# Optimization experiments

Hardware: AMD Instinct MI355X
Metric: run time of the kernel (lower is better)

## Reference

```python
import jax, jax.numpy as jnp
import numpy as np

B, N, D = 16, 512, 512
H, DH = 8, 64
INNER = H * DH            # attention inner dim = 512
FF = 4 * D                # feedforward hidden = 2048
CI = 2 * D                # conv expansion inner = 1024
K = 31                    # depthwise kernel
MAXPOS = 512
EPS = 1e-5                # LayerNorm / BatchNorm eps (torch defaults)
PAD = (K // 2, K // 2 - (K + 1) % 2)  # calc_same_padding(31) -> (15, 15)


def _ln(x, g, b):
    m = x.mean(-1, keepdims=True)
    v = ((x - m) ** 2).mean(-1, keepdims=True)
    return (x - m) / jnp.sqrt(v + EPS) * g + b


def _swish(x):
    return x * jax.nn.sigmoid(x)


def setup_inputs() -> dict:
    key = jax.random.key(0)
    ks = jax.random.split(key, 16)
    s = 0.02
    inp = {
        'x': jax.random.normal(ks[0], (B, N, D), jnp.float32),
        # FF1
        'ff1_ln_g': jnp.ones((D,), jnp.float32), 'ff1_ln_b': jnp.zeros((D,), jnp.float32),
        'ff1_w1': jax.random.normal(ks[1], (D, FF), jnp.float32) * s,
        'ff1_b1': jnp.zeros((FF,), jnp.float32),
        'ff1_w2': jax.random.normal(ks[2], (FF, D), jnp.float32) * s,
        'ff1_b2': jnp.zeros((D,), jnp.float32),
        # Attention
        'attn_ln_g': jnp.ones((D,), jnp.float32), 'attn_ln_b': jnp.zeros((D,), jnp.float32),
        'qkv_w': jax.random.normal(ks[3], (D, 3 * INNER), jnp.float32) * s,
        'out_w': jax.random.normal(ks[4], (INNER, D), jnp.float32) * s,
        'rel_emb': jax.random.normal(ks[5], (2 * MAXPOS + 1, DH), jnp.float32) * s,
        # Conv module
        'conv_ln_g': jnp.ones((D,), jnp.float32), 'conv_ln_b': jnp.zeros((D,), jnp.float32),
        'pw1_w': jax.random.normal(ks[6], (2 * CI, D), jnp.float32) * s,
        'pw1_b': jnp.zeros((2 * CI,), jnp.float32),
        'dw_w': jax.random.normal(ks[7], (CI, 1, K), jnp.float32) * s,
        'dw_b': jnp.zeros((CI,), jnp.float32),
        'bn_g': jnp.ones((CI,), jnp.float32), 'bn_b': jnp.zeros((CI,), jnp.float32),
        'bn_mean': jnp.zeros((CI,), jnp.float32), 'bn_var': jnp.ones((CI,), jnp.float32),
        'pw2_w': jax.random.normal(ks[8], (D, CI), jnp.float32) * s,
        'pw2_b': jnp.zeros((D,), jnp.float32),
        # FF2
        'ff2_ln_g': jnp.ones((D,), jnp.float32), 'ff2_ln_b': jnp.zeros((D,), jnp.float32),
        'ff2_w1': jax.random.normal(ks[9], (D, FF), jnp.float32) * s,
        'ff2_b1': jnp.zeros((FF,), jnp.float32),
        'ff2_w2': jax.random.normal(ks[10], (FF, D), jnp.float32) * s,
        'ff2_b2': jnp.zeros((D,), jnp.float32),
        # post norm
        'post_ln_g': jnp.ones((D,), jnp.float32), 'post_ln_b': jnp.zeros((D,), jnp.float32),
    }
    return inp


def _ff(x, g, b, w1, b1, w2, b2):
    h = _ln(x, g, b)
    h = _swish(h @ w1 + b1)
    return h @ w2 + b2


def _attention(x, g, b, qkv_w, out_w, rel_emb):
    n = x.shape[1]
    scale = DH ** (-0.5)
    h = _ln(x, g, b)
    qkv = h @ qkv_w                                    # [b,n,3*inner]
    q, k, v = jnp.split(qkv, 3, axis=-1)
    q = q.reshape(B, n, H, DH).transpose(0, 2, 1, 3)   # [b,h,n,d]
    k = k.reshape(B, n, H, DH).transpose(0, 2, 1, 3)
    v = v.reshape(B, n, H, DH).transpose(0, 2, 1, 3)
    dots = jnp.einsum('bhnd,bhmd->bhnm', q, k) * scale
    seq = jnp.arange(n)
    dist = jnp.clip(seq[:, None] - seq[None, :], -MAXPOS, MAXPOS) + MAXPOS  # [n,n]
    rpe = rel_emb[dist]                                # [n,r,d]
    pos = jnp.einsum('bhnd,nrd->bhnr', q, rpe) * scale
    sim = dots + pos
    attn = jax.nn.softmax(sim.astype(jnp.float32), axis=-1).astype(q.dtype)
    out = jnp.einsum('bhnm,bhmd->bhnd', attn, v)
    out = out.transpose(0, 2, 1, 3).reshape(B, n, INNER)
    return out @ out_w


def _conv_module(x, ln_g, ln_b, pw1_w, pw1_b, dw_w, dw_b, bn_g, bn_b, bn_mean, bn_var, pw2_w, pw2_b):
    h = _ln(x, ln_g, ln_b)                             # [b,n,c]
    h = h.transpose(0, 2, 1)                           # [b,c,n]
    h = jnp.einsum('oc,bcn->bon', pw1_w, h) + pw1_b[:, None]  # pointwise conv1 -> [b,2ci,n]
    out, gate = jnp.split(h, 2, axis=1)
    h = out * jax.nn.sigmoid(gate)                     # GLU -> [b,ci,n]
    h = jnp.pad(h, ((0, 0), (0, 0), PAD))
    h = jax.lax.conv_general_dilated(
        h, dw_w, window_strides=(1,), padding='VALID',
        feature_group_count=CI, dimension_numbers=('NCH', 'OIH', 'NCH'))
    h = h + dw_b[:, None]
    # BatchNorm1d eval-mode with running stats
    h = (h - bn_mean[:, None]) / jnp.sqrt(bn_var[:, None] + EPS) * bn_g[:, None] + bn_b[:, None]
    h = _swish(h)
    h = jnp.einsum('oc,bcn->bon', pw2_w, h) + pw2_b[:, None]  # pointwise conv2 -> [b,d,n]
    return h.transpose(0, 2, 1)


def reference(x, ff1_ln_g, ff1_ln_b, ff1_w1, ff1_b1, ff1_w2, ff1_b2,
              attn_ln_g, attn_ln_b, qkv_w, out_w, rel_emb,
              conv_ln_g, conv_ln_b, pw1_w, pw1_b, dw_w, dw_b,
              bn_g, bn_b, bn_mean, bn_var, pw2_w, pw2_b,
              ff2_ln_g, ff2_ln_b, ff2_w1, ff2_b1, ff2_w2, ff2_b2,
              post_ln_g, post_ln_b):
    x = 0.5 * _ff(x, ff1_ln_g, ff1_ln_b, ff1_w1, ff1_b1, ff1_w2, ff1_b2) + x
    x = _attention(x, attn_ln_g, attn_ln_b, qkv_w, out_w, rel_emb) + x
    x = _conv_module(x, conv_ln_g, conv_ln_b, pw1_w, pw1_b, dw_w, dw_b,
                     bn_g, bn_b, bn_mean, bn_var, pw2_w, pw2_b) + x
    x = 0.5 * _ff(x, ff2_ln_g, ff2_ln_b, ff2_w1, ff2_b1, ff2_w2, ff2_b2) + x
    return _ln(x, post_ln_g, post_ln_b)
```

## Files before the change

kernel.cpp:

```cpp
#include <hip/hip_runtime.h>
#include <stdint.h>

#define ROWS 8192
#define N_ 512

typedef __attribute__((ext_vector_type(4))) float f32x4;
typedef __attribute__((ext_vector_type(8))) short s16x8;
typedef __attribute__((ext_vector_type(4))) short s16x4;
typedef __attribute__((ext_vector_type(8))) unsigned short u16x8;

__device__ __forceinline__ float bf2f(unsigned short h){
  union { unsigned int u; float f; } v; v.u = ((unsigned int)h) << 16; return v.f;
}
__device__ __forceinline__ unsigned short f2bf(float f){
  union { float f; unsigned int u; } v; v.f = f;
  unsigned int r = v.u + 0x7FFFu + ((v.u >> 16) & 1u);
  return (unsigned short)(r >> 16);
}
__device__ __forceinline__ float sigm(float x){ return 1.f / (1.f + __expf(-x)); }
__device__ __forceinline__ unsigned cvtpk(float lo, float hi){
  unsigned r;
  asm("v_cvt_pk_bf16_f32 %0, %1, %2" : "=v"(r) : "v"(lo), "v"(hi));
  return r;
}

__global__ void k_transpose_cvt(const float* __restrict__ in, unsigned short* __restrict__ out,
                                int R, int C){
  __shared__ float t[32][33];
  int c0 = blockIdx.x*32, r0 = blockIdx.y*32;
  int tx = threadIdx.x & 31, ty = threadIdx.x >> 5;
  #pragma unroll
  for(int i=0;i<32;i+=8) t[ty+i][tx] = in[(size_t)(r0+ty+i)*C + c0+tx];
  __syncthreads();
  #pragma unroll
  for(int i=0;i<32;i+=8) out[(size_t)(c0+ty+i)*R + r0+tx] = f2bf(t[tx][ty+i]);
}

__global__ void k_cvt(const float* __restrict__ in, unsigned short* __restrict__ out, int n){
  int i = blockIdx.x*256 + threadIdx.x;
  if(i < n) out[i] = f2bf(in[i]);
}

__global__ void k_vtrans(const unsigned short* __restrict__ qkv, unsigned short* __restrict__ vt){
  __shared__ unsigned short t[64][72];
  const int tid = threadIdx.x;
  const int n0 = blockIdx.x * 64;
  const int bh = blockIdx.y;
  const int b = bh >> 3, h = bh & 7;
  #pragma unroll
  for(int i=0;i<2;i++){
    int flat = i*256 + tid;
    int tok = flat >> 3, c = flat & 7;
    u16x8 v = *(const u16x8*)(qkv + (size_t)(b*N_ + n0 + tok)*1536 + 1024 + h*64 + c*8);
    *(u16x8*)(&t[tok][c*8]) = v;
  }
  __syncthreads();
  #pragma unroll
  for(int i=0;i<2;i++){
    int flat = i*256 + tid;
    int d = flat >> 3, tc = flat & 7;
    u16x8 o;
    #pragma unroll
    for(int e=0;e<8;e++) o[e] = t[tc*8+e][d];
    *(u16x8*)(vt + (((size_t)bh*64 + d) << 9) + n0 + tc*8) = o;
  }
}

template<int OUTF32>
__global__ void k_ln(const float* __restrict__ x, const float* __restrict__ gw,
                     const float* __restrict__ bw, void* __restrict__ outp){
  const int row = blockIdx.x*4 + (threadIdx.x >> 6);
  const int lane = threadIdx.x & 63;
  const f32x4* xr = (const f32x4*)(x + (size_t)row*512);
  f32x4 v0 = xr[lane], v1 = xr[lane + 64];
  float s  = v0[0]+v0[1]+v0[2]+v0[3] + v1[0]+v1[1]+v1[2]+v1[3];
  float s2 = v0[0]*v0[0]+v0[1]*v0[1]+v0[2]*v0[2]+v0[3]*v0[3]
           + v1[0]*v1[0]+v1[1]*v1[1]+v1[2]*v1[2]+v1[3]*v1[3];
  #pragma unroll
  for(int off=1; off<64; off<<=1){ s += __shfl_xor(s, off); s2 += __shfl_xor(s2, off); }
  float mean = s * (1.f/512.f);
  float inv = rsqrtf(s2*(1.f/512.f) - mean*mean + 1e-5f);
  const f32x4* gv = (const f32x4*)gw; const f32x4* bv = (const f32x4*)bw;
  f32x4 g0 = gv[lane], g1 = gv[lane+64], b0 = bv[lane], b1 = bv[lane+64];
  f32x4 o0, o1;
  #pragma unroll
  for(int e=0;e<4;e++){ o0[e] = (v0[e]-mean)*inv*g0[e] + b0[e];
                        o1[e] = (v1[e]-mean)*inv*g1[e] + b1[e]; }
  if(OUTF32){
    f32x4* op = (f32x4*)((float*)outp + (size_t)row*512);
    op[lane] = o0; op[lane+64] = o1;
  } else {
    unsigned short* ob = (unsigned short*)outp + (size_t)row*512;
    s16x4 h0, h1;
    #pragma unroll
    for(int e=0;e<4;e++){ h0[e] = (short)f2bf(o0[e]); h1[e] = (short)f2bf(o1[e]); }
    *(s16x4*)(ob + lane*4) = h0;
    *(s16x4*)(ob + 256 + lane*4) = h1;
  }
}

template<int EPI>
__global__ __launch_bounds__(256, 2)
void k_gemm(const unsigned short* __restrict__ A, const unsigned short* __restrict__ Bt,
            const float* __restrict__ bias, const float* __restrict__ res,
            void* __restrict__ outp, int M, int N, int K){
  __shared__ unsigned short As[128*64];
  __shared__ unsigned short Bs[128*64];
  const int tid = threadIdx.x, lane = tid & 63, wave = tid >> 6;
  const int nwg = gridDim.x * gridDim.y;
  int orig = blockIdx.x + gridDim.x * blockIdx.y;
  int q8 = nwg >> 3, r8 = nwg & 7, xcd = orig & 7, idx = orig >> 3;
  int wg = (xcd < r8 ? xcd * (q8 + 1) : r8 * (q8 + 1) + (xcd - r8) * q8) + idx;
  const int m0 = (wg / gridDim.x) * 128, n0 = (wg % gridDim.x) * 128;
  const int wm = (wave >> 1) * 64, wn = (wave & 1) * 64;
  f32x4 acc[4][4];
  #pragma unroll
  for(int a=0;a<4;a++)
    #pragma unroll
    for(int b=0;b<4;b++) acc[a][b] = (f32x4){0.f,0.f,0.f,0.f};

  for(int kt = 0; kt < K; kt += 64){
    #pragma unroll
    for(int i=0;i<4;i++){
      int flat = i*256 + tid;
      int r = flat >> 3, c = flat & 7;
      int dst = r*64 + ((c ^ (r & 7)) << 3);
      *(u16x8*)(&As[dst]) = *(const u16x8*)(A + (size_t)(m0 + r)*K + kt + c*8);
      *(u16x8*)(&Bs[dst]) = *(const u16x8*)(Bt + (size_t)(n0 + r)*K + kt + c*8);
    }
    __syncthreads();
    #pragma unroll
    for(int ks=0; ks<2; ks++){
      s16x8 af[4], bfr[4];
      #pragma unroll
      for(int mi=0;mi<4;mi++){
        int row = wm + mi*16 + (lane & 15);
        int ch = (ks*4 + (lane >> 4)) ^ (row & 7);
        af[mi] = *(const s16x8*)(&As[row*64 + ch*8]);
      }
      #pragma unroll
      for(int ni=0;ni<4;ni++){
        int row = wn + ni*16 + (lane & 15);
        int ch = (ks*4 + (lane >> 4)) ^ (row & 7);
        bfr[ni] = *(const s16x8*)(&Bs[row*64 + ch*8]);
      }
      #pragma unroll
      for(int mi=0;mi<4;mi++)
        #pragma unroll
        for(int ni=0;ni<4;ni++)
          acc[mi][ni] = __builtin_amdgcn_mfma_f32_16x16x32_bf16(af[mi], bfr[ni], acc[mi][ni], 0, 0, 0);
    }
    __syncthreads();
  }
  const int rb = (lane >> 4) * 4, cb = lane & 15;
  #pragma unroll
  for(int mi=0;mi<4;mi++){
    #pragma unroll
    for(int ni=0;ni<4;ni++){
      int col = n0 + wn + ni*16 + cb;
      #pragma unroll
      for(int r=0;r<4;r++){
        int row = m0 + wm + mi*16 + rb + r;
        float v = acc[mi][ni][r];
        if(EPI==1||EPI==2||EPI==4||EPI==5) v += bias[col];
        if(EPI==2) v = 0.5f*v + res[(size_t)row*N + col];
        if(EPI==3||EPI==5) v += res[(size_t)row*N + col];
        if(EPI==1) v = v * sigm(v);
        if(EPI==0||EPI==1||EPI==4) ((unsigned short*)outp)[(size_t)row*N + col] = f2bf(v);
        else                        ((float*)outp)[(size_t)row*N + col] = v;
      }
    }
  }
}

__global__ __launch_bounds__(256, 2)
void k_attn(const unsigned short* __restrict__ qkv, const unsigned short* __restrict__ vt,
            const unsigned short* __restrict__ emb, unsigned short* __restrict__ outb){
  __shared__ unsigned short KV[512*64];
  const int tid = threadIdx.x, lane = tid & 63, w = tid >> 6;
  const int q0 = blockIdx.x * 64, h = blockIdx.y, b = blockIdx.z;
  const int j = lane & 15, g = lane >> 4;
  const int n0w = q0 + w*16;
  const size_t qkvbase = (size_t)b*N_*1536;

  #pragma unroll
  for(int i=0;i<16;i++){
    int flat = i*256 + tid;
    int r = flat >> 3, c = flat & 7;
    *(u16x8*)(&KV[r*64 + ((c ^ (r & 7)) << 3)]) =
      *(const u16x8*)(qkv + qkvbase + (size_t)r*1536 + 512 + h*64 + c*8);
  }
  s16x8 qf[2];
  #pragma unroll
  for(int ks=0;ks<2;ks++)
    qf[ks] = *(const s16x8*)(qkv + qkvbase + (size_t)(n0w + j)*1536 + h*64 + ks*32 + g*8);
  f32x4 pa1 = {0.f,0.f,0.f,0.f};
  #pragma unroll
  for(int ks=0;ks<2;ks++){
    s16x8 e1 = *(const s16x8*)(emb + (size_t)(n0w + 513 + j)*64 + ks*32 + g*8);
    pa1 = __builtin_amdgcn_mfma_f32_16x16x32_bf16(e1, qf[ks], pa1, 0,0,0);
  }
  __syncthreads();

  f32x4 sc[32];
  #pragma unroll
  for(int rt=0;rt<32;rt++){
    const int cb = n0w - rt*16 + 512;
    f32x4 s   = {0.f,0.f,0.f,0.f};
    f32x4 pa0 = {0.f,0.f,0.f,0.f};
    #pragma unroll
    for(int ks=0;ks<2;ks++){
      int row = rt*16 + j;
      int ch = (ks*4 + g) ^ (row & 7);
      s16x8 kf = *(const s16x8*)(&KV[row*64 + (ch<<3)]);
      s = __builtin_amdgcn_mfma_f32_16x16x32_bf16(kf, qf[ks], s, 0,0,0);
      s16x8 e0 = *(const s16x8*)(emb + (size_t)(cb - 15 + j)*64 + ks*32 + g*8);
      pa0 = __builtin_amdgcn_mfma_f32_16x16x32_bf16(e0, qf[ks], pa0, 0,0,0);
    }
    #pragma unroll
    for(int reg=0;reg<4;reg++){
      int elem = (j + 3 - reg) & 3;
      float s0 = (elem & 2) ? ((elem & 1) ? pa0[3] : pa0[2]) : ((elem & 1) ? pa0[1] : pa0[0]);
      float s1 = (elem & 2) ? ((elem & 1) ? pa1[3] : pa1[2]) : ((elem & 1) ? pa1[1] : pa1[0]);
      int m = j + 15 - g*4 - reg;
      int src = j + (((m & 15) >> 2) << 4);
      float v0 = __shfl(s0, src);
      float v1 = __shfl(s1, src);
      sc[rt][reg] = s[reg] + (m < 16 ? v0 : v1);
    }
    pa1 = pa0;
  }
  __syncthreads();

  #pragma unroll
  for(int i=0;i<16;i++){
    int flat = i*256 + tid;
    int d = flat >> 6, rc = flat & 63;
    u16x8 v = *(const u16x8*)(vt + (((size_t)(b*8 + h)*64 + d) << 9) + rc*8);
    *(u16x8*)(&KV[d*512 + ((rc ^ (d & 7)) << 3)]) = v;
  }

  const float C2 = 0.125f * 1.4426950408889634f;
  float mx = -1e30f;
  #pragma unroll
  for(int rt=0;rt<32;rt++)
    mx = fmaxf(mx, fmaxf(fmaxf(sc[rt][0], sc[rt][1]), fmaxf(sc[rt][2], sc[rt][3])));
  mx = fmaxf(mx, __shfl_xor(mx, 16));
  mx = fmaxf(mx, __shfl_xor(mx, 32));
  const float mc = mx * C2;
  float sm = 0.f;
  unsigned w0[32], w1[32];
  #pragma unroll
  for(int rt=0;rt<32;rt++){
    float p0 = exp2f(fmaf(sc[rt][0], C2, -mc));
    float p1 = exp2f(fmaf(sc[rt][1], C2, -mc));
    float p2 = exp2f(fmaf(sc[rt][2], C2, -mc));
    float p3 = exp2f(fmaf(sc[rt][3], C2, -mc));
    sm += (p0 + p1) + (p2 + p3);
    w0[rt] = cvtpk(p0, p1);
    w1[rt] = cvtpk(p2, p3);
  }
  sm += __shfl_xor(sm, 16);
  sm += __shfl_xor(sm, 32);
  float inv = 1.f / sm;
  __syncthreads();

  f32x4 o[4];
  #pragma unroll
  for(int dt=0;dt<4;dt++) o[dt] = (f32x4){0.f,0.f,0.f,0.f};
  const int srcA = j + ((g & 1) << 5);
  const int srcB = srcA + 16;
  const bool hi = (g >= 2);
  #pragma unroll
  for(int rts=0; rts<16; rts++){
    unsigned a0 = __shfl(w0[2*rts],   srcA);
    unsigned a1 = __shfl(w1[2*rts],   srcA);
    unsigned a2 = __shfl(w0[2*rts],   srcB);
    unsigned a3 = __shfl(w1[2*rts],   srcB);
    unsigned b0 = __shfl(w0[2*rts+1], srcA);
    unsigned b1 = __shfl(w1[2*rts+1], srcA);
    unsigned b2 = __shfl(w0[2*rts+1], srcB);
    unsigned b3 = __shfl(w1[2*rts+1], srcB);
    union { unsigned u[4]; s16x8 v; } pu;
    pu.u[0] = hi ? b0 : a0;
    pu.u[1] = hi ? b1 : a1;
    pu.u[2] = hi ? b2 : a2;
    pu.u[3] = hi ? b3 : a3;
    #pragma unroll
    for(int dt=0;dt<4;dt++){
      int d = dt*16 + j;
      int ch = (rts*4 + g) ^ (d & 7);
      s16x8 vf = *(const s16x8*)(&KV[d*512 + (ch<<3)]);
      o[dt] = __builtin_amdgcn_mfma_f32_16x16x32_bf16(pu.v, vf, o[dt], 0,0,0);
    }
  }
  #pragma unroll
  for(int reg=0;reg<4;reg++){
    float invq = __shfl(inv, (g<<2) + reg);
    int tok = n0w + (g<<2) + reg;
    #pragma unroll
    for(int dt=0;dt<4;dt++)
      outb[(size_t)(b*N_ + tok)*512 + h*64 + dt*16 + j] = f2bf(o[dt][reg] * invq);
  }
}

__global__ void k_glu(const unsigned short* __restrict__ hid, unsigned short* __restrict__ outp){
  size_t i = (size_t)blockIdx.x*256 + threadIdx.x;
  int row = (int)(i >> 7), cc = (int)(i & 127);
  u16x8 a  = *(const u16x8*)(hid + (size_t)row*2048 + cc*8);
  u16x8 gt = *(const u16x8*)(hid + (size_t)row*2048 + 1024 + cc*8);
  u16x8 o;
  #pragma unroll
  for(int e=0;e<8;e++){
    float av = bf2f(a[e]), gv = bf2f(gt[e]);
    o[e] = f2bf(av * sigm(gv));
  }
  *(u16x8*)(outp + (size_t)row*1024 + cc*8) = o;
}

__global__ __launch_bounds__(256, 2)
void k_dwconv(const unsigned short* __restrict__ gin, const float* __restrict__ dww,
              const float* __restrict__ dwb, const float* __restrict__ bng,
              const float* __restrict__ bnb, const float* __restrict__ bnm,
              const float* __restrict__ bnv, unsigned short* __restrict__ outp){
  __shared__ unsigned short gl[94][136];
  __shared__ float wl[31][128];
  const int c0 = blockIdx.x*128, n0 = blockIdx.y*64, b = blockIdx.z;
  const int tid = threadIdx.x;
  for(int i=0;i<6;i++){
    int flat = i*256 + tid;
    if(flat < 94*16){
      int r = flat >> 4, c = flat & 15;
      int n = n0 - 15 + r;
      u16x8 v = {0,0,0,0,0,0,0,0};
      if(n >= 0 && n < 512) v = *(const u16x8*)(gin + (size_t)(b*512 + n)*1024 + c0 + c*8);
      *(u16x8*)(&gl[r][c*8]) = v;
    }
  }
  for(int i=0;i<16;i++){
    int flat = i*256 + tid;
    if(flat < 31*128){
      int t = flat >> 7, cc = flat & 127;
      wl[t][cc] = dww[(size_t)(c0 + cc)*31 + t];
    }
  }
  __syncthreads();
  const int tc = tid & 31, tn = tid >> 5;
  f32x4 acc[8];
  #pragma unroll
  for(int nn=0;nn<8;nn++) acc[nn] = (f32x4){0.f,0.f,0.f,0.f};
  for(int t=0;t<31;t++){
    f32x4 wv = *(const f32x4*)(&wl[t][tc*4]);
    #pragma unroll
    for(int nn=0;nn<8;nn++){
      s16x4 gv = *(const s16x4*)(&gl[tn*8 + nn + t][tc*4]);
      f32x4 g4 = { bf2f((unsigned short)gv[0]), bf2f((unsigned short)gv[1]),
                   bf2f((unsigned short)gv[2]), bf2f((unsigned short)gv[3]) };
      acc[nn] += g4 * wv;
    }
  }
  #pragma unroll
  for(int e=0;e<4;e++){
    int c = c0 + tc*4 + e;
    float s  = bng[c] * rsqrtf(bnv[c] + 1e-5f);
    float sh = bnb[c] - bnm[c]*s;
    float db = dwb[c];
    #pragma unroll
    for(int nn=0;nn<8;nn++){
      float v = (acc[nn][e] + db)*s + sh;
      v = v * sigm(v);
      outp[(size_t)(b*512 + n0 + tn*8 + nn)*1024 + c] = f2bf(v);
    }
  }
}

extern "C" void kernel_launch(void* const* d_in, const int* in_sizes, int n_in,
                              void* d_out, int out_size, void* d_ws, size_t ws_size,
                              hipStream_t stream){
  const float* x        = (const float*)d_in[0];
  const float* ff1_ln_g = (const float*)d_in[1];
  const float* ff1_ln_b = (const float*)d_in[2];
  const float* ff1_w1   = (const float*)d_in[3];
  const float* ff1_b1   = (const float*)d_in[4];
  const float* ff1_w2   = (const float*)d_in[5];
  const float* ff1_b2   = (const float*)d_in[6];
  const float* attn_ln_g= (const float*)d_in[7];
  const float* attn_ln_b= (const float*)d_in[8];
  const float* qkv_w    = (const float*)d_in[9];
  const float* out_w    = (const float*)d_in[10];
  const float* rel_emb  = (const float*)d_in[11];
  const float* conv_ln_g= (const float*)d_in[12];
  const float* conv_ln_b= (const float*)d_in[13];
  const float* pw1_w    = (const float*)d_in[14];
  const float* pw1_b    = (const float*)d_in[15];
  const float* dw_w     = (const float*)d_in[16];
  const float* dw_b     = (const float*)d_in[17];
  const float* bn_g     = (const float*)d_in[18];
  const float* bn_b     = (const float*)d_in[19];
  const float* bn_mean  = (const float*)d_in[20];
  const float* bn_var   = (const float*)d_in[21];
  const float* pw2_w    = (const float*)d_in[22];
  const float* pw2_b    = (const float*)d_in[23];
  const float* ff2_ln_g = (const float*)d_in[24];
  const float* ff2_ln_b = (const float*)d_in[25];
  const float* ff2_w1   = (const float*)d_in[26];
  const float* ff2_b1   = (const float*)d_in[27];
  const float* ff2_w2   = (const float*)d_in[28];
  const float* ff2_b2   = (const float*)d_in[29];
  const float* post_ln_g= (const float*)d_in[30];
  const float* post_ln_b= (const float*)d_in[31];
  (void)in_sizes; (void)n_in; (void)out_size; (void)ws_size;

  char* ws = (char*)d_ws;
  size_t off = 0;
  auto alloc = [&](size_t bytes)->char*{ char* p = ws + off; off += (bytes + 255) & ~(size_t)255; return p; };
  float*          res  = (float*)         alloc((size_t)ROWS*512*4);
  unsigned short* hbuf = (unsigned short*)alloc((size_t)ROWS*512*2);
  unsigned short* hid  = (unsigned short*)alloc((size_t)ROWS*2048*2);
  unsigned short* qkvb = (unsigned short*)alloc((size_t)ROWS*1536*2);
  unsigned short* glub = (unsigned short*)alloc((size_t)ROWS*1024*2);
  unsigned short* attnout = glub;
  unsigned short* dwout   = qkvb;
  unsigned short* vtb     = hid;
  unsigned short* w1t  = (unsigned short*)alloc((size_t)2048*512*2);
  unsigned short* w2t  = (unsigned short*)alloc((size_t)2048*512*2);
  unsigned short* qkvt = (unsigned short*)alloc((size_t)1536*512*2);
  unsigned short* outt = (unsigned short*)alloc((size_t)512*512*2);
  unsigned short* pw1c = (unsigned short*)alloc((size_t)2048*512*2);
  unsigned short* pw2c = (unsigned short*)alloc((size_t)512*1024*2);
  unsigned short* f2w1t= (unsigned short*)alloc((size_t)2048*512*2);
  unsigned short* f2w2t= (unsigned short*)alloc((size_t)2048*512*2);
  unsigned short* rele = (unsigned short*)alloc((size_t)1025*64*2);

  k_transpose_cvt<<<dim3(64, 16), 256, 0, stream>>>(ff1_w1, w1t, 512, 2048);
  k_transpose_cvt<<<dim3(16, 64), 256, 0, stream>>>(ff1_w2, w2t, 2048, 512);
  k_transpose_cvt<<<dim3(48, 16), 256, 0, stream>>>(qkv_w, qkvt, 512, 1536);
  k_transpose_cvt<<<dim3(16, 16), 256, 0, stream>>>(out_w, outt, 512, 512);
  k_transpose_cvt<<<dim3(64, 16), 256, 0, stream>>>(ff2_w1, f2w1t, 512, 2048);
  k_transpose_cvt<<<dim3(16, 64), 256, 0, stream>>>(ff2_w2, f2w2t, 2048, 512);
  k_cvt<<<2048*512/256, 256, 0, stream>>>(pw1_w, pw1c, 2048*512);
  k_cvt<<<512*1024/256, 256, 0, stream>>>(pw2_w, pw2c, 512*1024);
  k_cvt<<<(1025*64+255)/256, 256, 0, stream>>>(rel_emb, rele, 1025*64);

  k_ln<0><<<ROWS/4, 256, 0, stream>>>(x, ff1_ln_g, ff1_ln_b, hbuf);
  k_gemm<1><<<dim3(16, 64), 256, 0, stream>>>(hbuf, w1t, ff1_b1, nullptr, hid, ROWS, 2048, 512);
  k_gemm<2><<<dim3(4, 64), 256, 0, stream>>>(hid, w2t, ff1_b2, x, res, ROWS, 512, 2048);
  k_ln<0><<<ROWS/4, 256, 0, stream>>>(res, attn_ln_g, attn_ln_b, hbuf);
  k_gemm<0><<<dim3(12, 64), 256, 0, stream>>>(hbuf, qkvt, nullptr, nullptr, qkvb, ROWS, 1536, 512);
  k_vtrans<<<dim3(8, 128), 256, 0, stream>>>(qkvb, vtb);
  k_attn<<<dim3(8, 8, 16), 256, 0, stream>>>(qkvb, vtb, rele, attnout);
  k_gemm<3><<<dim3(4, 64), 256, 0, stream>>>(attnout, outt, nullptr, res, res, ROWS, 512, 512);
  k_ln<0><<<ROWS/4, 256, 0, stream>>>(res, conv_ln_g, conv_ln_b, hbuf);
  k_gemm<4><<<dim3(16, 64), 256, 0, stream>>>(hbuf, pw1c, pw1_b, nullptr, hid, ROWS, 2048, 512);
  k_glu<<<ROWS*128/256, 256, 0, stream>>>(hid, glub);
  k_dwconv<<<dim3(8, 8, 16), 256, 0, stream>>>(glub, dw_w, dw_b, bn_g, bn_b, bn_mean, bn_var, dwout);
  k_gemm<5><<<dim3(4, 64), 256, 0, stream>>>(dwout, pw2c, pw2_b, res, res, ROWS, 512, 1024);
  k_ln<0><<<ROWS/4, 256, 0, stream>>>(res, ff2_ln_g, ff2_ln_b, hbuf);
  k_gemm<1><<<dim3(16, 64), 256, 0, stream>>>(hbuf, f2w1t, ff2_b1, nullptr, hid, ROWS, 2048, 512);
  k_gemm<2><<<dim3(4, 64), 256, 0, stream>>>(hid, f2w2t, ff2_b2, res, res, ROWS, 512, 2048);
  k_ln<1><<<ROWS/4, 256, 0, stream>>>(res, post_ln_g, post_ln_b, d_out);
}
```

Measured before the change: 506.5 us.

## Use direct global-to-LDS loads, fuse V transpose into QKV GEMM, widen attention blocks

GEMM and attention tile loads now use global_load_lds so data goes straight into LDS without passing through registers, with the XOR swizzle moved to the source address. The QKV projection GEMM gets a new epilogue that writes the V columns already transposed into the vt buffer, which removes the separate k_vtrans kernel and its extra pass over V. Attention blocks grow to 512 threads covering 128 queries each, so every K/V tile staged in LDS is shared by twice as many queries. The risks are the transposed V epilogue making strided 8-byte stores and the larger attention blocks changing occupancy.

New measurement: 580.0 us. 1.15x slower.

```diff
diff --git a/kernel.cpp b/kernel.cpp
--- a/kernel.cpp
+++ b/kernel.cpp
@@ -7,6 +7,7 @@
 typedef __attribute__((ext_vector_type(4))) float f32x4;
 typedef __attribute__((ext_vector_type(8))) short s16x8;
 typedef __attribute__((ext_vector_type(4))) short s16x4;
+typedef __attribute__((ext_vector_type(4))) unsigned short u16x4;
 typedef __attribute__((ext_vector_type(8))) unsigned short u16x8;
 
 __device__ __forceinline__ float bf2f(unsigned short h){
@@ -23,6 +24,11 @@
   asm("v_cvt_pk_bf16_f32 %0, %1, %2" : "=v"(r) : "v"(lo), "v"(hi));
   return r;
 }
+__device__ __forceinline__ void gload16(const void* g, void* l){
+  __builtin_amdgcn_global_load_lds(
+    (const __attribute__((address_space(1))) void*)g,
+    (__attribute__((address_space(3))) void*)l, 16, 0, 0);
+}
 
 __global__ void k_transpose_cvt(const float* __restrict__ in, unsigned short* __restrict__ out,
                                 int R, int C){
@@ -39,31 +45,6 @@
 __global__ void k_cvt(const float* __restrict__ in, unsigned short* __restrict__ out, int n){
   int i = blockIdx.x*256 + threadIdx.x;
   if(i < n) out[i] = f2bf(in[i]);
-}
-
-__global__ void k_vtrans(const unsigned short* __restrict__ qkv, unsigned short* __restrict__ vt){
-  __shared__ unsigned short t[64][72];
-  const int tid = threadIdx.x;
-  const int n0 = blockIdx.x * 64;
-  const int bh = blockIdx.y;
-  const int b = bh >> 3, h = bh & 7;
-  #pragma unroll
-  for(int i=0;i<2;i++){
-    int flat = i*256 + tid;
-    int tok = flat >> 3, c = flat & 7;
-    u16x8 v = *(const u16x8*)(qkv + (size_t)(b*N_ + n0 + tok)*1536 + 1024 + h*64 + c*8);
-    *(u16x8*)(&t[tok][c*8]) = v;
-  }
-  __syncthreads();
-  #pragma unroll
-  for(int i=0;i<2;i++){
-    int flat = i*256 + tid;
-    int d = flat >> 3, tc = flat & 7;
-    u16x8 o;
-    #pragma unroll
-    for(int e=0;e<8;e++) o[e] = t[tc*8+e][d];
-    *(u16x8*)(vt + (((size_t)bh*64 + d) << 9) + n0 + tc*8) = o;
-  }
 }
 
 template<int OUTF32>
@@ -103,9 +84,9 @@
 __global__ __launch_bounds__(256, 2)
 void k_gemm(const unsigned short* __restrict__ A, const unsigned short* __restrict__ Bt,
             const float* __restrict__ bias, const float* __restrict__ res,
-            void* __restrict__ outp, int M, int N, int K){
-  __shared__ unsigned short As[128*64];
-  __shared__ unsigned short Bs[128*64];
+            void* __restrict__ outp, unsigned short* __restrict__ vt, int M, int N, int K){
+  __shared__ alignas(16) unsigned short As[128*64];
+  __shared__ alignas(16) unsigned short Bs[128*64];
   const int tid = threadIdx.x, lane = tid & 63, wave = tid >> 6;
   const int nwg = gridDim.x * gridDim.y;
   int orig = blockIdx.x + gridDim.x * blockIdx.y;
@@ -123,10 +104,10 @@
     #pragma unroll
     for(int i=0;i<4;i++){
       int flat = i*256 + tid;
-      int r = flat >> 3, c = flat & 7;
-      int dst = r*64 + ((c ^ (r & 7)) << 3);
-      *(u16x8*)(&As[dst]) = *(const u16x8*)(A + (size_t)(m0 + r)*K + kt + c*8);
-      *(u16x8*)(&Bs[dst]) = *(const u16x8*)(Bt + (size_t)(n0 + r)*K + kt + c*8);
+      int r = flat >> 3;
+      int cs = ((flat & 7) ^ (r & 7)) << 3;
+      gload16(A  + (size_t)(m0 + r)*K + kt + cs, &As[flat*8]);
+      gload16(Bt + (size_t)(n0 + r)*K + kt + cs, &Bs[flat*8]);
     }
     __syncthreads();
     #pragma unroll
@@ -158,37 +139,46 @@
     #pragma unroll
     for(int ni=0;ni<4;ni++){
       int col = n0 + wn + ni*16 + cb;
-      #pragma unroll
-      for(int r=0;r<4;r++){
-        int row = m0 + wm + mi*16 + rb + r;
-        float v = acc[mi][ni][r];
-        if(EPI==1||EPI==2||EPI==4||EPI==5) v += bias[col];
-        if(EPI==2) v = 0.5f*v + res[(size_t)row*N + col];
-        if(EPI==3||EPI==5) v += res[(size_t)row*N + col];
-        if(EPI==1) v = v * sigm(v);
-        if(EPI==0||EPI==1||EPI==4) ((unsigned short*)outp)[(size_t)row*N + col] = f2bf(v);
-        else                        ((float*)outp)[(size_t)row*N + col] = v;
+      int rowbase = m0 + wm + mi*16 + rb;
+      if(EPI==6 && col >= 1024){
+        u16x4 tv;
+        #pragma unroll
+        for(int r=0;r<4;r++) tv[r] = f2bf(acc[mi][ni][r]);
+        int bb = rowbase >> 9, n = rowbase & 511;
+        *(u16x4*)(vt + (((size_t)(bb*512 + col - 1024)) << 9) + n) = tv;
+      } else {
+        #pragma unroll
+        for(int r=0;r<4;r++){
+          int row = rowbase + r;
+          float v = acc[mi][ni][r];
+          if(EPI==1||EPI==2||EPI==4||EPI==5) v += bias[col];
+          if(EPI==2) v = 0.5f*v + res[(size_t)row*N + col];
+          if(EPI==3||EPI==5) v += res[(size_t)row*N + col];
+          if(EPI==1) v = v * sigm(v);
+          if(EPI==0||EPI==1||EPI==4||EPI==6) ((unsigned short*)outp)[(size_t)row*N + col] = f2bf(v);
+          else                               ((float*)outp)[(size_t)row*N + col] = v;
+        }
       }
     }
   }
 }
 
-__global__ __launch_bounds__(256, 2)
+__global__ __launch_bounds__(512, 4)
 void k_attn(const unsigned short* __restrict__ qkv, const unsigned short* __restrict__ vt,
             const unsigned short* __restrict__ emb, unsigned short* __restrict__ outb){
-  __shared__ unsigned short KV[512*64];
+  __shared__ alignas(16) unsigned short KV[512*64];
   const int tid = threadIdx.x, lane = tid & 63, w = tid >> 6;
-  const int q0 = blockIdx.x * 64, h = blockIdx.y, b = blockIdx.z;
+  const int q0 = blockIdx.x * 128, h = blockIdx.y, b = blockIdx.z;
   const int j = lane & 15, g = lane >> 4;
   const int n0w = q0 + w*16;
   const size_t qkvbase = (size_t)b*N_*1536;
 
   #pragma unroll
-  for(int i=0;i<16;i++){
-    int flat = i*256 + tid;
-    int r = flat >> 3, c = flat & 7;
-    *(u16x8*)(&KV[r*64 + ((c ^ (r & 7)) << 3)]) =
-      *(const u16x8*)(qkv + qkvbase + (size_t)r*1536 + 512 + h*64 + c*8);
+  for(int i=0;i<8;i++){
+    int flat = i*512 + tid;
+    int r = flat >> 3;
+    int cs = ((flat & 7) ^ (r & 7)) << 3;
+    gload16(qkv + qkvbase + (size_t)r*1536 + 512 + h*64 + cs, &KV[flat*8]);
   }
   s16x8 qf[2];
   #pragma unroll
@@ -233,11 +223,11 @@
   __syncthreads();
 
   #pragma unroll
-  for(int i=0;i<16;i++){
-    int flat = i*256 + tid;
-    int d = flat >> 6, rc = flat & 63;
-    u16x8 v = *(const u16x8*)(vt + (((size_t)(b*8 + h)*64 + d) << 9) + rc*8);
-    *(u16x8*)(&KV[d*512 + ((rc ^ (d & 7)) << 3)]) = v;
+  for(int i=0;i<8;i++){
+    int flat = i*512 + tid;
+    int d = flat >> 6;
+    int rcs = ((flat & 63) ^ (d & 7)) << 3;
+    gload16(vt + (((size_t)(b*8 + h)*64 + d) << 9) + rcs, &KV[flat*8]);
   }
 
   const float C2 = 0.125f * 1.4426950408889634f;
@@ -443,20 +433,19 @@
   k_cvt<<<(1025*64+255)/256, 256, 0, stream>>>(rel_emb, rele, 1025*64);
 
   k_ln<0><<<ROWS/4, 256, 0, stream>>>(x, ff1_ln_g, ff1_ln_b, hbuf);
-  k_gemm<1><<<dim3(16, 64), 256, 0, stream>>>(hbuf, w1t, ff1_b1, nullptr, hid, ROWS, 2048, 512);
-  k_gemm<2><<<dim3(4, 64), 256, 0, stream>>>(hid, w2t, ff1_b2, x, res, ROWS, 512, 2048);
+  k_gemm<1><<<dim3(16, 64), 256, 0, stream>>>(hbuf, w1t, ff1_b1, nullptr, hid, nullptr, ROWS, 2048, 512);
+  k_gemm<2><<<dim3(4, 64), 256, 0, stream>>>(hid, w2t, ff1_b2, x, res, nullptr, ROWS, 512, 2048);
   k_ln<0><<<ROWS/4, 256, 0, stream>>>(res, attn_ln_g, attn_ln_b, hbuf);
-  k_gemm<0><<<dim3(12, 64), 256, 0, stream>>>(hbuf, qkvt, nullptr, nullptr, qkvb, ROWS, 1536, 512);
-  k_vtrans<<<dim3(8, 128), 256, 0, stream>>>(qkvb, vtb);
-  k_attn<<<dim3(8, 8, 16), 256, 0, stream>>>(qkvb, vtb, rele, attnout);
-  k_gemm<3><<<dim3(4, 64), 256, 0, stream>>>(attnout, outt, nullptr, res, res, ROWS, 512, 512);
+  k_gemm<6><<<dim3(12, 64), 256, 0, stream>>>(hbuf, qkvt, nullptr, nullptr, qkvb, vtb, ROWS, 1536, 512);
+  k_attn<<<dim3(4, 8, 16), 512, 0, stream>>>(qkvb, vtb, rele, attnout);
+  k_gemm<3><<<dim3(4, 64), 256, 0, stream>>>(attnout, outt, nullptr, res, res, nullptr, ROWS, 512, 512);
   k_ln<0><<<ROWS/4, 256, 0, stream>>>(res, conv_ln_g, conv_ln_b, hbuf);
-  k_gemm<4><<<dim3(16, 64), 256, 0, stream>>>(hbuf, pw1c, pw1_b, nullptr, hid, ROWS, 2048, 512);
+  k_gemm<4><<<dim3(16, 64), 256, 0, stream>>>(hbuf, pw1c, pw1_b, nullptr, hid, nullptr, ROWS, 2048, 512);
   k_glu<<<ROWS*128/256, 256, 0, stream>>>(hid, glub);
   k_dwconv<<<dim3(8, 8, 16), 256, 0, stream>>>(glub, dw_w, dw_b, bn_g, bn_b, bn_mean, bn_var, dwout);
-  k_gemm<5><<<dim3(4, 64), 256, 0, stream>>>(dwout, pw2c, pw2_b, res, res, ROWS, 512, 1024);
+  k_gemm<5><<<dim3(4, 64), 256, 0, stream>>>(dwout, pw2c, pw2_b, res, res, nullptr, ROWS, 512, 1024);
   k_ln<0><<<ROWS/4, 256, 0, stream>>>(res, ff2_ln_g, ff2_ln_b, hbuf);
-  k_gemm<1><<<dim3(16, 64), 256, 0, stream>>>(hbuf, f2w1t, ff2_b1, nullptr, hid, ROWS, 2048, 512);
-  k_gemm<2><<<dim3(4, 64), 256, 0, stream>>>(hid, f2w2t, ff2_b2, res, res, ROWS, 512, 2048);
+  k_gemm<1><<<dim3(16, 64), 256, 0, stream>>>(hbuf, f2w1t, ff2_b1, nullptr, hid, nullptr, ROWS, 2048, 512);
+  k_gemm<2><<<dim3(4, 64), 256, 0, stream>>>(hid, f2w2t, ff2_b2, res, res, nullptr, ROWS, 512, 2048);
   k_ln<1><<<ROWS/4, 256, 0, stream>>>(res, post_ln_g, post_ln_b, d_out);
 }
```
